# Optimization experiments

Hardware: AMD Instinct MI355X
Metric: run time of the kernel (lower is better)

## Reference

```python
import jax, jax.numpy as jnp
import numpy as np

NQ = 14      # num_qubits
DEPTH = 6    # ansatz depth
DIM = 2 ** NQ

# Convention: flattened statevector index uses qubit 0 as the MOST significant bit
# (qubit q sits at bit position NQ-1-q). This matches building the state by
# successive kron with later qubits in lower bits.

def _bits(idx, q):
    return (idx >> (NQ - 1 - q)) & 1


def setup_inputs() -> dict:
    key = jax.random.key(0)
    k1, k2, k3 = jax.random.split(key, 3)
    x = jax.random.normal(k1, (512, NQ), dtype=jnp.float32)
    theta = jax.random.normal(k2, (NQ * DEPTH,), dtype=jnp.float32) * 0.1
    head_w = jax.random.normal(k3, (2, NQ), dtype=jnp.float32) * 0.3
    head_b = jnp.zeros((2,), dtype=jnp.float32)
    return {"x": x, "theta": theta, "head_w": head_w, "head_b": head_b}


def _simulate(x, theta):
    B = x.shape[0]
    half = 0.5 * x
    c = jnp.cos(half).astype(jnp.complex64)          # (B, NQ)
    s = jnp.sin(half).astype(jnp.complex64)
    # RX(x_q) applied to |0>^n gives a product state: kron of [cos(x/2), -i sin(x/2)]
    state = jnp.ones((B, 1), dtype=jnp.complex64)
    for q in range(NQ):
        v = jnp.stack([c[:, q], (-1j) * s[:, q]], axis=-1)   # (B, 2)
        state = (state[:, :, None] * v[:, None, :]).reshape(B, -1)
    # state: (B, DIM)

    idx = jnp.arange(DIM)
    bits = jnp.stack([_bits(idx, q) for q in range(NQ)], axis=0)     # (NQ, DIM)
    # CZ chain on (q, q+1): diagonal phase (-1)^(sum of adjacent bit ANDs)
    cz_parity = jnp.sum(bits[:-1] * bits[1:], axis=0) % 2
    cz_sign = jnp.where(cz_parity == 1, -1.0, 1.0).astype(jnp.complex64)  # (DIM,)

    for d in range(DEPTH):
        for q in range(NQ):
            t = 0.5 * theta[d * NQ + q]
            ct, st = jnp.cos(t), jnp.sin(t)
            G = jnp.stack([jnp.stack([ct, -st]), jnp.stack([st, ct])]).astype(jnp.complex64)
            sr = state.reshape(B, 2 ** q, 2, -1)   # qubit q at this axis
            state = jnp.einsum('ab,iqbr->iqar', G, sr).reshape(B, DIM)
        state = state * cz_sign[None, :]

    probs = state.real ** 2 + state.imag ** 2       # (B, DIM)
    zsign = (1.0 - 2.0 * bits).astype(jnp.float32)  # (NQ, DIM), Z eigenvalues per qubit
    zexp = probs @ zsign.T                          # (B, NQ), index = our qubit label
    # Qiskit: observable i = 'I'*i + 'Z' + 'I'*(NQ-i-1) acts on qubit NQ-1-i
    return zexp[:, ::-1]


def reference(x, theta, head_w, head_b):
    exp_tensor = _simulate(x, theta)                # (B, NQ)
    logits = exp_tensor @ head_w.T + head_b         # (B, 2)
    return logits
```

## Files before the change

### kernel.cpp

```cpp
#include <hip/hip_runtime.h>
#include <math.h>

#define NQ 14
#define DEPTH 6
#define BLOCK 512
#define TS 528u
#define BUFSZ 33792u

typedef _Float16 h16;
typedef h16 h4 __attribute__((ext_vector_type(4)));
typedef float f4 __attribute__((ext_vector_type(4)));

#define BAR_WAR() asm volatile("s_barrier" ::: "memory")
#define BAR_PUB() asm volatile("s_waitcnt lgkmcnt(0)\n\ts_barrier" ::: "memory")

__global__ __launch_bounds__(512, 1) void prep_kernel(
    const float* __restrict__ theta, const float* __restrict__ head_w,
    h16* __restrict__ BmG, float* __restrict__ wtab, float* __restrict__ outp)
{
  __shared__ float2 gtab[DEPTH * NQ];
  const int t = threadIdx.x;
  if (t < 256)
    *(float4*)(outp + 4 * t) = make_float4(0.f, 0.f, 0.f, 0.f);
  if (t < DEPTH * NQ) {
    int d = t / NQ, bit = t - d * NQ;
    float hg = 0.5f * theta[d * NQ + (13 - bit)];
    gtab[t] = make_float2(cosf(hg), sinf(hg));
  }
  if (t < 88) {
    int o, v; float s = 0.f;
    if (t < 32) { o = t >> 4; v = t & 15;
      #pragma unroll
      for (int i = 0; i < 4; ++i) s += ((v>>i)&1) ? -head_w[o*NQ+i] : head_w[o*NQ+i];
    } else if (t < 64) { o = (t-32) >> 4; v = t & 15;
      #pragma unroll
      for (int i = 0; i < 4; ++i) s += ((v>>i)&1) ? -head_w[o*NQ+8+i] : head_w[o*NQ+8+i];
    } else if (t < 72) { o = (t-64) >> 2; v = t & 3;
      s = ((v&1)?-head_w[o*NQ+4]:head_w[o*NQ+4]) + ((v&2)?-head_w[o*NQ+5]:head_w[o*NQ+5]);
    } else if (t < 80) { o = (t-72) >> 2; v = t & 3;
      s = ((v&1)?-head_w[o*NQ+6]:head_w[o*NQ+6]) + ((v&2)?-head_w[o*NQ+7]:head_w[o*NQ+7]);
    } else { o = (t-80) >> 2; v = t & 3;
      s = ((v&1)?-head_w[o*NQ+12]:head_w[o*NQ+12]) + ((v&2)?-head_w[o*NQ+13]:head_w[o*NQ+13]);
    }
    wtab[t] = s;
  }
  __syncthreads();
  #pragma unroll
  for (int i = 0; i < 12; ++i) {
    int e = t + (i << 9);
    int pid = e >> 8, n = (e >> 4) & 15, k = e & 15;
    int d = pid >> 2, p = pid & 3;
    float val;
    if (p < 3) {
      val = 1.f;
      #pragma unroll
      for (int j = 0; j < 4; ++j) {
        float2 g = gtab[d * NQ + 4 * p + j];
        val *= ((n >> j) & 1) ? (((k >> j) & 1) ? g.x : g.y)
                              : (((k >> j) & 1) ? -g.y : g.x);
      }
      if (d >= 1) {
        int s = ((k & (k >> 1)) ^ ((k >> 1) & (k >> 2)) ^ ((k >> 2) & (k >> 3))) & 1;
        if (s) val = -val;
        if ((n & 1) && (k & 8)) val = -val;
      }
    } else {
      if ((((n ^ k) >> 2) & 3) != 0) val = 0.f;
      else {
        float2 gA = gtab[d * NQ + 12], gB = gtab[d * NQ + 13];
        float f0 = (n & 1) ? ((k & 1) ? gA.x : gA.y) : ((k & 1) ? -gA.y : gA.x);
        float f1 = ((n >> 1) & 1) ? (((k >> 1) & 1) ? gB.x : gB.y)
                                  : (((k >> 1) & 1) ? -gB.y : gB.x);
        val = f0 * f1;
        if (d >= 1 && (k & (k >> 1) & 1)) val = -val;
      }
    }
    BmG[pid * 256 + n * 16 + k] = (h16)val;
  }
}

__global__ __launch_bounds__(BLOCK, 8) void qsim_kernel(
    const float* __restrict__ x, const h16* __restrict__ BmG,
    const float* __restrict__ wtabG, const float* __restrict__ head_b,
    float* __restrict__ out)
{
  extern __shared__ __align__(16) char sbuf[];
  __shared__ float wtab[88];
  __shared__ float xc[NQ], xs[NQ];
  __shared__ float redbuf[16];

  const int t = threadIdx.x;
  const int b = blockIdx.x >> 1;
  const int comp = blockIdx.x & 1;
  const int lane = t & 63;
  const int w = t >> 6;
  const int m = lane & 15;
  const int kg = lane >> 4;

  if (t < 88) wtab[t] = wtabG[t];
  if (t >= 128 && t < 128 + NQ) {
    int bit = t - 128;
    float h = 0.5f * x[b * NQ + (13 - bit)];
    xc[bit] = cosf(h); xs[bit] = sinf(h);
  }
  __syncthreads();

  {
    float Mt = 1.f;
    #pragma unroll
    for (int p = 5; p < 14; ++p) Mt *= ((t >> (p - 5)) & 1) ? xs[p] : xc[p];
    const int pct = __popc((unsigned)t);
    uint32_t base = (uint32_t)(t >> 3) * TS + (uint32_t)((2 * t) & 15) * 32;
    #pragma unroll
    for (int g = 0; g < 4; ++g) {
      union { h16 h[8]; uint4 u; } pk;
      #pragma unroll
      for (int i = 0; i < 8; ++i) {
        int j = g * 8 + i;
        float mm = Mt;
        #pragma unroll
        for (int p = 0; p < 5; ++p) mm *= ((j >> p) & 1) ? xs[p] : xc[p];
        int e = (pct + __popc((unsigned)j)) & 3;
        float v = (comp == 0) ? ((e == 0) ? mm : ((e == 2) ? -mm : 0.f))
                              : ((e == 1) ? -mm : ((e == 3) ? mm : 0.f));
        pk.h[i] = (h16)v;
      }
      *(uint4*)(sbuf + base + (uint32_t)(g >> 1) * 32 + (uint32_t)(g & 1) * 16) = pk.u;
    }
  }
  __syncthreads();

  const uint32_t raA = (uint32_t)w * (8 * TS) + (uint32_t)m * 32 + (uint32_t)kg * 8;
  const uint32_t raB = (uint32_t)((w & 1) * 8 + 16 * (w >> 1)) * TS
                     + (uint32_t)m * 32 + (uint32_t)kg * 8;
  const uint32_t wbase = (uint32_t)m * TS + ((uint32_t)(w >> 1) + 4u * (uint32_t)kg) * 32
                       + (uint32_t)((w & 1) * 16);

  float l0 = 0.f, l1 = 0.f;

  auto do_half = [&](uint32_t rbase, h4 gB, h4 gA, bool last) {
    h4 av[8];
    #pragma unroll
    for (int jt = 0; jt < 8; ++jt)
      av[jt] = *(const h4*)(sbuf + rbase + (uint32_t)jt * TS);
    uint32_t qk[8][2];
    float bs0 = 0.f, bs1 = 0.f;
    if (last) {
      bs0 = wtab[32 + m] + wtab[64 + (w >> 1)] + wtab[72 + kg];
      bs1 = wtab[48 + m] + wtab[68 + (w >> 1)] + wtab[76 + kg];
    }
    __builtin_amdgcn_s_setprio(1);
    #pragma unroll
    for (int jt = 0; jt < 8; ++jt) {
      f4 acc = {0.f, 0.f, 0.f, 0.f};
      acc = __builtin_amdgcn_mfma_f32_16x16x16f16(av[jt], gB, acc, 0, 0, 0);
      union { h16 h[4]; h4 v; uint32_t d[2]; } c1;
      c1.h[0] = (h16)acc[0]; c1.h[1] = (h16)acc[1];
      c1.h[2] = (h16)acc[2]; c1.h[3] = (h16)acc[3];
      f4 acc2 = {0.f, 0.f, 0.f, 0.f};
      acc2 = __builtin_amdgcn_mfma_f32_16x16x16f16(gA, c1.v, acc2, 0, 0, 0);
      if (!last) {
        union { h16 h[4]; uint32_t d[2]; } c2;
        c2.h[0] = (h16)acc2[0]; c2.h[1] = (h16)acc2[1];
        c2.h[2] = (h16)acc2[2]; c2.h[3] = (h16)acc2[3];
        qk[jt][0] = c2.d[0]; qk[jt][1] = c2.d[1];
      } else {
        float wt0 = wtab[(w & 1) * 8 + jt], wt1 = wtab[16 + (w & 1) * 8 + jt];
        #pragma unroll
        for (int j = 0; j < 4; ++j) {
          float pr = acc2[j] * acc2[j];
          l0 += pr * (bs0 + wt0 + wtab[80 + j]);
          l1 += pr * (bs1 + wt1 + wtab[84 + j]);
        }
      }
    }
    __builtin_amdgcn_s_setprio(0);
    if (!last) {
      BAR_WAR();
      #pragma unroll
      for (int r = 0; r < 4; ++r) {
        uint32_t o[4];
        #pragma unroll
        for (int q = 0; q < 4; ++q) {
          uint32_t lo = qk[2 * q][r >> 1], hi = qk[2 * q + 1][r >> 1];
          o[q] = (r & 1) ? __builtin_amdgcn_perm(hi, lo, 0x07060302u)
                         : __builtin_amdgcn_perm(hi, lo, 0x05040100u);
        }
        *(uint4*)(sbuf + wbase + (uint32_t)r * (16 * TS)) =
            make_uint4(o[0], o[1], o[2], o[3]);
      }
      BAR_PUB();
    }
  };

  const h16* fb = BmG + (m * 16 + kg * 4);

  #pragma unroll 1
  for (int d = 0; d < DEPTH; ++d) {
    const h16* nf = fb + d * 1024;
    h4 g0f = *(const h4*)(nf +   0);
    h4 g1f = *(const h4*)(nf + 256);
    h4 g2f = *(const h4*)(nf + 512);
    h4 g3f = *(const h4*)(nf + 768);
    do_half(raA, g0f, g1f, false);
    do_half(raB, g2f, g3f, d == DEPTH - 1);
  }

  #pragma unroll
  for (int off = 32; off > 0; off >>= 1) {
    l0 += __shfl_xor(l0, off);
    l1 += __shfl_xor(l1, off);
  }
  if (lane == 0) { redbuf[w] = l0; redbuf[8 + w] = l1; }
  __syncthreads();
  if (t == 0) {
    float s0 = 0.f, s1 = 0.f;
    #pragma unroll
    for (int i = 0; i < 8; ++i) { s0 += redbuf[i]; s1 += redbuf[8 + i]; }
    if (comp == 0) { s0 += head_b[0]; s1 += head_b[1]; }
    atomicAdd(&out[b * 2 + 0], s0);
    atomicAdd(&out[b * 2 + 1], s1);
  }
}

extern "C" void kernel_launch(void* const* d_in, const int* in_sizes, int n_in,
                              void* d_out, int out_size, void* d_ws, size_t ws_size,
                              hipStream_t stream) {
    const float* x      = (const float*)d_in[0];
    const float* theta  = (const float*)d_in[1];
    const float* head_w = (const float*)d_in[2];
    const float* head_b = (const float*)d_in[3];
    float* outp = (float*)d_out;
    h16*  BmG   = (h16*)d_ws;
    float* wtabG = (float*)((char*)d_ws + 12288);
    const int batch = in_sizes[0] / NQ;
    prep_kernel<<<1, 512, 0, stream>>>(theta, head_w, BmG, wtabG, outp);
    qsim_kernel<<<batch * 2, BLOCK, BUFSZ, stream>>>(x, BmG, wtabG, head_b, outp);
}
```

Baseline: 51.71 us.

## Merge real and imaginary component blocks into one block per sample

Each block now handles both the real and imaginary parts of one sample's statevector, holding two LDS buffers, instead of launching two blocks per sample. The kernel can then write the output directly instead of using atomicAdd, so prep_kernel no longer zeroes the output. In exchange each block uses twice the shared memory and more registers, and launch_bounds occupancy drops from 8 to 4. There are half as many blocks and barriers, but each block does twice the MFMA work per barrier.

```diff
diff --git a/kernel.cpp b/kernel.cpp
--- a/kernel.cpp
+++ b/kernel.cpp
@@ -16,12 +16,10 @@
 
 __global__ __launch_bounds__(512, 1) void prep_kernel(
     const float* __restrict__ theta, const float* __restrict__ head_w,
-    h16* __restrict__ BmG, float* __restrict__ wtab, float* __restrict__ outp)
+    h16* __restrict__ BmG, float* __restrict__ wtab)
 {
   __shared__ float2 gtab[DEPTH * NQ];
   const int t = threadIdx.x;
-  if (t < 256)
-    *(float4*)(outp + 4 * t) = make_float4(0.f, 0.f, 0.f, 0.f);
   if (t < DEPTH * NQ) {
     int d = t / NQ, bit = t - d * NQ;
     float hg = 0.5f * theta[d * NQ + (13 - bit)];
@@ -79,7 +77,7 @@
   }
 }
 
-__global__ __launch_bounds__(BLOCK, 8) void qsim_kernel(
+__global__ __launch_bounds__(BLOCK, 4) void qsim_kernel(
     const float* __restrict__ x, const h16* __restrict__ BmG,
     const float* __restrict__ wtabG, const float* __restrict__ head_b,
     float* __restrict__ out)
@@ -90,12 +88,14 @@
   __shared__ float redbuf[16];
 
   const int t = threadIdx.x;
-  const int b = blockIdx.x >> 1;
-  const int comp = blockIdx.x & 1;
+  const int b = blockIdx.x;
   const int lane = t & 63;
   const int w = t >> 6;
   const int m = lane & 15;
   const int kg = lane >> 4;
+
+  char* const bufR = sbuf;
+  char* const bufI = sbuf + BUFSZ;
 
   if (t < 88) wtab[t] = wtabG[t];
   if (t >= 128 && t < 128 + NQ) {
@@ -113,7 +113,7 @@
     uint32_t base = (uint32_t)(t >> 3) * TS + (uint32_t)((2 * t) & 15) * 32;
     #pragma unroll
     for (int g = 0; g < 4; ++g) {
-      union { h16 h[8]; uint4 u; } pk;
+      union { h16 h[8]; uint4 u; } pkR, pkI;
       #pragma unroll
       for (int i = 0; i < 8; ++i) {
         int j = g * 8 + i;
@@ -121,11 +121,12 @@
         #pragma unroll
         for (int p = 0; p < 5; ++p) mm *= ((j >> p) & 1) ? xs[p] : xc[p];
         int e = (pct + __popc((unsigned)j)) & 3;
-        float v = (comp == 0) ? ((e == 0) ? mm : ((e == 2) ? -mm : 0.f))
-                              : ((e == 1) ? -mm : ((e == 3) ? mm : 0.f));
-        pk.h[i] = (h16)v;
-      }
-      *(uint4*)(sbuf + base + (uint32_t)(g >> 1) * 32 + (uint32_t)(g & 1) * 16) = pk.u;
+        pkR.h[i] = (h16)((e == 0) ? mm : ((e == 2) ? -mm : 0.f));
+        pkI.h[i] = (h16)((e == 1) ? -mm : ((e == 3) ? mm : 0.f));
+      }
+      uint32_t off = base + (uint32_t)(g >> 1) * 32 + (uint32_t)(g & 1) * 16;
+      *(uint4*)(bufR + off) = pkR.u;
+      *(uint4*)(bufI + off) = pkI.u;
     }
   }
   __syncthreads();
@@ -139,11 +140,14 @@
   float l0 = 0.f, l1 = 0.f;
 
   auto do_half = [&](uint32_t rbase, h4 gB, h4 gA, bool last) {
-    h4 av[8];
+    h4 avR[8], avI[8];
     #pragma unroll
     for (int jt = 0; jt < 8; ++jt)
-      av[jt] = *(const h4*)(sbuf + rbase + (uint32_t)jt * TS);
-    uint32_t qk[8][2];
+      avR[jt] = *(const h4*)(bufR + rbase + (uint32_t)jt * TS);
+    #pragma unroll
+    for (int jt = 0; jt < 8; ++jt)
+      avI[jt] = *(const h4*)(bufI + rbase + (uint32_t)jt * TS);
+    uint32_t qkR[8][2], qkI[8][2];
     float bs0 = 0.f, bs1 = 0.f;
     if (last) {
       bs0 = wtab[32 + m] + wtab[64 + (w >> 1)] + wtab[72 + kg];
@@ -153,8 +157,8 @@
     #pragma unroll
     for (int jt = 0; jt < 8; ++jt) {
       f4 acc = {0.f, 0.f, 0.f, 0.f};
-      acc = __builtin_amdgcn_mfma_f32_16x16x16f16(av[jt], gB, acc, 0, 0, 0);
-      union { h16 h[4]; h4 v; uint32_t d[2]; } c1;
+      acc = __builtin_amdgcn_mfma_f32_16x16x16f16(avR[jt], gB, acc, 0, 0, 0);
+      union { h16 h[4]; h4 v; } c1;
       c1.h[0] = (h16)acc[0]; c1.h[1] = (h16)acc[1];
       c1.h[2] = (h16)acc[2]; c1.h[3] = (h16)acc[3];
       f4 acc2 = {0.f, 0.f, 0.f, 0.f};
@@ -163,7 +167,7 @@
         union { h16 h[4]; uint32_t d[2]; } c2;
         c2.h[0] = (h16)acc2[0]; c2.h[1] = (h16)acc2[1];
         c2.h[2] = (h16)acc2[2]; c2.h[3] = (h16)acc2[3];
-        qk[jt][0] = c2.d[0]; qk[jt][1] = c2.d[1];
+        qkR[jt][0] = c2.d[0]; qkR[jt][1] = c2.d[1];
       } else {
         float wt0 = wtab[(w & 1) * 8 + jt], wt1 = wtab[16 + (w & 1) * 8 + jt];
         #pragma unroll
@@ -174,20 +178,48 @@
         }
       }
     }
+    #pragma unroll
+    for (int jt = 0; jt < 8; ++jt) {
+      f4 acc = {0.f, 0.f, 0.f, 0.f};
+      acc = __builtin_amdgcn_mfma_f32_16x16x16f16(avI[jt], gB, acc, 0, 0, 0);
+      union { h16 h[4]; h4 v; } c1;
+      c1.h[0] = (h16)acc[0]; c1.h[1] = (h16)acc[1];
+      c1.h[2] = (h16)acc[2]; c1.h[3] = (h16)acc[3];
+      f4 acc2 = {0.f, 0.f, 0.f, 0.f};
+      acc2 = __builtin_amdgcn_mfma_f32_16x16x16f16(gA, c1.v, acc2, 0, 0, 0);
+      if (!last) {
+        union { h16 h[4]; uint32_t d[2]; } c2;
+        c2.h[0] = (h16)acc2[0]; c2.h[1] = (h16)acc2[1];
+        c2.h[2] = (h16)acc2[2]; c2.h[3] = (h16)acc2[3];
+        qkI[jt][0] = c2.d[0]; qkI[jt][1] = c2.d[1];
+      } else {
+        float wt0 = wtab[(w & 1) * 8 + jt], wt1 = wtab[16 + (w & 1) * 8 + jt];
+        #pragma unroll
+        for (int j = 0; j < 4; ++j) {
+          float pr = acc2[j] * acc2[j];
+          l0 += pr * (bs0 + wt0 + wtab[80 + j]);
+          l1 += pr * (bs1 + wt1 + wtab[84 + j]);
+        }
+      }
+    }
     __builtin_amdgcn_s_setprio(0);
     if (!last) {
       BAR_WAR();
       #pragma unroll
       for (int r = 0; r < 4; ++r) {
-        uint32_t o[4];
+        uint32_t oR[4], oI[4];
         #pragma unroll
         for (int q = 0; q < 4; ++q) {
-          uint32_t lo = qk[2 * q][r >> 1], hi = qk[2 * q + 1][r >> 1];
-          o[q] = (r & 1) ? __builtin_amdgcn_perm(hi, lo, 0x07060302u)
-                         : __builtin_amdgcn_perm(hi, lo, 0x05040100u);
+          uint32_t loR = qkR[2 * q][r >> 1], hiR = qkR[2 * q + 1][r >> 1];
+          uint32_t loI = qkI[2 * q][r >> 1], hiI = qkI[2 * q + 1][r >> 1];
+          oR[q] = (r & 1) ? __builtin_amdgcn_perm(hiR, loR, 0x07060302u)
+                          : __builtin_amdgcn_perm(hiR, loR, 0x05040100u);
+          oI[q] = (r & 1) ? __builtin_amdgcn_perm(hiI, loI, 0x07060302u)
+                          : __builtin_amdgcn_perm(hiI, loI, 0x05040100u);
         }
-        *(uint4*)(sbuf + wbase + (uint32_t)r * (16 * TS)) =
-            make_uint4(o[0], o[1], o[2], o[3]);
+        uint32_t wa = wbase + (uint32_t)r * (16 * TS);
+        *(uint4*)(bufR + wa) = make_uint4(oR[0], oR[1], oR[2], oR[3]);
+        *(uint4*)(bufI + wa) = make_uint4(oI[0], oI[1], oI[2], oI[3]);
       }
       BAR_PUB();
     }
@@ -214,12 +246,11 @@
   if (lane == 0) { redbuf[w] = l0; redbuf[8 + w] = l1; }
   __syncthreads();
   if (t == 0) {
-    float s0 = 0.f, s1 = 0.f;
+    float s0 = head_b[0], s1 = head_b[1];
     #pragma unroll
     for (int i = 0; i < 8; ++i) { s0 += redbuf[i]; s1 += redbuf[8 + i]; }
-    if (comp == 0) { s0 += head_b[0]; s1 += head_b[1]; }
-    atomicAdd(&out[b * 2 + 0], s0);
-    atomicAdd(&out[b * 2 + 1], s1);
+    out[b * 2 + 0] = s0;
+    out[b * 2 + 1] = s1;
   }
 }
 
@@ -234,6 +265,6 @@
     h16*  BmG   = (h16*)d_ws;
     float* wtabG = (float*)((char*)d_ws + 12288);
     const int batch = in_sizes[0] / NQ;
-    prep_kernel<<<1, 512, 0, stream>>>(theta, head_w, BmG, wtabG, outp);
-    qsim_kernel<<<batch * 2, BLOCK, BUFSZ, stream>>>(x, BmG, wtabG, head_b, outp);
+    prep_kernel<<<1, 512, 0, stream>>>(theta, head_w, BmG, wtabG);
+    qsim_kernel<<<batch, BLOCK, 2 * BUFSZ, stream>>>(x, BmG, wtabG, head_b, outp);
 }
```

New measurement: 52.79 us. 2.1% more time.
